# Optimization experiments

Hardware: AMD Instinct MI355X
Metric: run time of the kernel (lower is better)

## Reference

```python
import jax, jax.numpy as jnp
import numpy as np

# model geometry (matches init_kwargs cfg)
D = 768        # D_EMB
PATCH = 16
T = 8192
N = T // PATCH # 512 patch tokens
H = 12         # heads
HD = D // H    # 64 head dim
NL = 6         # layers
DFF = 4 * D
B = 8
LN_EPS = 1e-5


def setup_inputs() -> dict:
    key = jax.random.key(0)
    ks = iter(jax.random.split(key, 32))
    def g(shape, scale=0.02):
        return jax.random.normal(next(ks), shape, jnp.float32) * scale
    return dict(
        x=jax.random.normal(next(ks), (B, T), jnp.float32),
        pp_w=g((D, PATCH)), pp_b=jnp.zeros((D,), jnp.float32),
        pe=g((N, D)),
        ln1_g=jnp.ones((NL, D), jnp.float32), ln1_b=jnp.zeros((NL, D), jnp.float32),
        qkv_w=g((NL, 3 * D, D)), out_w=g((NL, D, D)),
        ln2_g=jnp.ones((NL, D), jnp.float32), ln2_b=jnp.zeros((NL, D), jnp.float32),
        fc1_w=g((NL, DFF, D)), fc2_w=g((NL, D, DFF)),
        lnf_g=jnp.ones((D,), jnp.float32), lnf_b=jnp.zeros((D,), jnp.float32),
        h1_w=g((D // 2, D)), h1_b=jnp.zeros((D // 2,), jnp.float32),
        h2_w=g((2, D // 2)), h2_b=jnp.zeros((2,), jnp.float32),
    )


def _ln(x, g, b):
    m = x.mean(-1, keepdims=True)
    v = ((x - m) ** 2).mean(-1, keepdims=True)
    return (x - m) / jnp.sqrt(v + LN_EPS) * g + b


def reference(x, pp_w, pp_b, pe, ln1_g, ln1_b, qkv_w, out_w,
              ln2_g, ln2_b, fc1_w, fc2_w, lnf_g, lnf_b,
              h1_w, h1_b, h2_w, h2_b):
    Bx = x.shape[0]
    # patch embed: [B, N, PATCH] @ W^T + b -> [B, N, D]
    z = jnp.einsum('bnp,dp->bnd', x[:, :N * PATCH].reshape(Bx, N, PATCH), pp_w) + pp_b
    z = z + pe  # positional embedding (arange indexes whole table)
    mask = jnp.tril(jnp.ones((N, N), dtype=bool))
    for i in range(NL):
        # --- attention (manual causal softmax, dropout=eval/no-op) ---
        h = _ln(z, ln1_g[i], ln1_b[i])
        qkv = jnp.einsum('bnd,ed->bne', h, qkv_w[i])            # [B,N,3D]
        qkv = qkv.reshape(Bx, N, 3, H, HD).transpose(2, 0, 3, 1, 4)
        q, k, v = qkv[0], qkv[1], qkv[2]                         # [B,H,N,HD]
        s = jnp.einsum('bhld,bhmd->bhlm', q, k) / np.sqrt(HD)
        s = jnp.where(mask, s, -jnp.inf)
        a = jax.nn.softmax(s, axis=-1)
        o = jnp.einsum('bhlm,bhmd->bhld', a, v)
        o = o.transpose(0, 2, 1, 3).reshape(Bx, N, D)
        z = z + jnp.einsum('bnd,ed->bne', o, out_w[i])
        # --- FFN (exact gelu, matching F.gelu default) ---
        h = _ln(z, ln2_g[i], ln2_b[i])
        f = jax.nn.gelu(jnp.einsum('bnd,fd->bnf', h, fc1_w[i]), approximate=False)
        z = z + jnp.einsum('bnf,df->bnd', f, fc2_w[i])
    enc = _ln(z, lnf_g, lnf_b).mean(axis=1)                      # [B, D]
    y = jax.nn.relu(enc @ h1_w.T + h1_b)
    return y @ h2_w.T + h2_b                                     # [B, 2]
```

## Files before the change

### kernel.cpp

```cpp
#include <hip/hip_runtime.h>
#include <hip/hip_bf16.h>
#include <math.h>

#define D_EMB 768
#define NPATCH 16
#define NTOK 512
#define NHEAD 12
#define HDIM 64
#define NLAYER 6
#define DFF 3072
#define BATCH 8
#define MTOK (BATCH * NTOK)

typedef __attribute__((ext_vector_type(8))) short bf16x8;
typedef __attribute__((ext_vector_type(4))) float f32x4;

__device__ __forceinline__ float bf2f(ushort s) {
    unsigned u = ((unsigned)s) << 16;
    return __builtin_bit_cast(float, u);
}
__device__ __forceinline__ ushort f2bf(float f) {
    unsigned u = __builtin_bit_cast(unsigned, f);
    unsigned r = (u + 0x7FFFu + ((u >> 16) & 1u)) >> 16;
    return (ushort)r;
}

__global__ __launch_bounds__(256)
void f2bf4_kernel(const float* __restrict__ s0, ushort* __restrict__ d0, int n0,
                  const float* __restrict__ s1, ushort* __restrict__ d1, int n1,
                  const float* __restrict__ s2, ushort* __restrict__ d2, int n2,
                  const float* __restrict__ s3, ushort* __restrict__ d3, int n3)
{
    int i = blockIdx.x * 256 + threadIdx.x;
    const float* s; ushort* d; int off;
    if (i < n0)                { s = s0; d = d0; off = i; }
    else if (i < n0 + n1)      { s = s1; d = d1; off = i - n0; }
    else if (i < n0 + n1 + n2) { s = s2; d = d2; off = i - n0 - n1; }
    else if (i < n0 + n1 + n2 + n3) { s = s3; d = d3; off = i - n0 - n1 - n2; }
    else return;
    float4 v = *(const float4*)(s + (size_t)off * 4);
    ushort4 o;
    o.x = f2bf(v.x); o.y = f2bf(v.y); o.z = f2bf(v.z); o.w = f2bf(v.w);
    *(ushort4*)(d + (size_t)off * 4) = o;
}

__global__ __launch_bounds__(256)
void patch_embed_kernel(const float* __restrict__ x, const float* __restrict__ pw,
                        const float* __restrict__ pb, const float* __restrict__ pe,
                        float* __restrict__ z)
{
    int bn = blockIdx.x;
    int b = bn >> 9, n = bn & 511;
    __shared__ float xs[NPATCH];
    int t = threadIdx.x;
    if (t < NPATCH) xs[t] = x[(size_t)b * 8192 + n * NPATCH + t];
    __syncthreads();
    for (int d = t; d < D_EMB; d += 256) {
        float acc = pb[d] + pe[(size_t)n * D_EMB + d];
        const float* w = pw + (size_t)d * NPATCH;
        #pragma unroll
        for (int p = 0; p < NPATCH; ++p) acc += xs[p] * w[p];
        z[(size_t)bn * D_EMB + d] = acc;
    }
}

__device__ __forceinline__ float block_reduce_sum_256(float v)
{
    __shared__ float lds[4];
    #pragma unroll
    for (int o = 32; o > 0; o >>= 1) v += __shfl_xor(v, o);
    int lane = threadIdx.x & 63, wid = threadIdx.x >> 6;
    __syncthreads();
    if (lane == 0) lds[wid] = v;
    __syncthreads();
    return lds[0] + lds[1] + lds[2] + lds[3];
}

__device__ __forceinline__ void store_val(float* p, float v)  { *p = v; }
__device__ __forceinline__ void store_val(ushort* p, float v) { *p = f2bf(v); }

template<typename OT>
__global__ __launch_bounds__(256)
void ln_kernel(const float* __restrict__ x, const float* __restrict__ g,
               const float* __restrict__ bta, OT* __restrict__ y)
{
    int row = blockIdx.x;
    const float* xr = x + (size_t)row * D_EMB;
    int t = threadIdx.x;
    float vals[3];
    float s = 0.f;
    #pragma unroll
    for (int i = 0; i < 3; ++i) { vals[i] = xr[t + i * 256]; s += vals[i]; }
    float mean = block_reduce_sum_256(s) * (1.0f / D_EMB);
    float ss = 0.f;
    #pragma unroll
    for (int i = 0; i < 3; ++i) { float d = vals[i] - mean; ss += d * d; }
    float var = block_reduce_sum_256(ss) * (1.0f / D_EMB);
    float rstd = rsqrtf(var + 1e-5f);
    #pragma unroll
    for (int i = 0; i < 3; ++i) {
        int d = t + i * 256;
        store_val(y + (size_t)row * D_EMB + d, (vals[i] - mean) * rstd * g[d] + bta[d]);
    }
}

template<typename OT>
__global__ __launch_bounds__(256)
void reduce_ln_kernel(const float* __restrict__ pbuf, float* __restrict__ z,
                      const float* __restrict__ g, const float* __restrict__ bta,
                      OT* __restrict__ y)
{
    int row = blockIdx.x;
    int t = threadIdx.x;
    const float* p0 = pbuf + (size_t)row * D_EMB;
    const float* p1 = pbuf + (size_t)MTOK * D_EMB + (size_t)row * D_EMB;
    float* zr = z + (size_t)row * D_EMB;
    float vals[3];
    float s = 0.f;
    #pragma unroll
    for (int i = 0; i < 3; ++i) {
        int d = t + i * 256;
        float v = zr[d] + p0[d] + p1[d];
        vals[i] = v;
        zr[d] = v;
        s += v;
    }
    float mean = block_reduce_sum_256(s) * (1.0f / D_EMB);
    float ss = 0.f;
    #pragma unroll
    for (int i = 0; i < 3; ++i) { float d = vals[i] - mean; ss += d * d; }
    float var = block_reduce_sum_256(ss) * (1.0f / D_EMB);
    float rstd = rsqrtf(var + 1e-5f);
    #pragma unroll
    for (int i = 0; i < 3; ++i) {
        int d = t + i * 256;
        store_val(y + (size_t)row * D_EMB + d, (vals[i] - mean) * rstd * g[d] + bta[d]);
    }
}

#define STAGE64(buf, k0)                                                           \
    {                                                                              \
        _Pragma("unroll")                                                          \
        for (int j = 0; j < 2; ++j) {                                              \
            int row = j * 32 + srow;                                               \
            int lcol = pcol ^ (row & 7);                                           \
            const ushort* sa = Ab + (size_t)(bm + row) * lda + (k0) + (lcol << 3); \
            __builtin_amdgcn_global_load_lds(                                      \
                (const __attribute__((address_space(1))) unsigned int*)sa,         \
                (__attribute__((address_space(3))) unsigned int*)&As[buf][row * 64 + (pcol << 3)], \
                16, 0, 0);                                                         \
        }                                                                          \
        _Pragma("unroll")                                                          \
        for (int j = 0; j < 4; ++j) {                                              \
            int row = j * 32 + srow;                                               \
            int lcol = pcol ^ (row & 7);                                           \
            const ushort* sb = Wb + (size_t)(bn + row) * lda + (k0) + (lcol << 3); \
            __builtin_amdgcn_global_load_lds(                                      \
                (const __attribute__((address_space(1))) unsigned int*)sb,         \
                (__attribute__((address_space(3))) unsigned int*)&Bs[buf][row * 64 + (pcol << 3)], \
                16, 0, 0);                                                         \
        }                                                                          \
    }

#define COMPUTE64(buf)                                                             \
    {                                                                              \
        _Pragma("unroll")                                                          \
        for (int kk = 0; kk < 2; ++kk) {                                           \
            int c = kk * 4 + lg;                                                   \
            bf16x8 a[4], b[2];                                                     \
            _Pragma("unroll")                                                      \
            for (int m = 0; m < 4; ++m) {                                          \
                int row = m * 16 + lr;                                             \
                a[m] = *(const bf16x8*)(&As[buf][row * 64 + ((c ^ (row & 7)) << 3)]); \
            }                                                                      \
            _Pragma("unroll")                                                      \
            for (int n = 0; n < 2; ++n) {                                          \
                int row = w * 32 + n * 16 + lr;                                    \
                b[n] = *(const bf16x8*)(&Bs[buf][row * 64 + ((c ^ (row & 7)) << 3)]); \
            }                                                                      \
            _Pragma("unroll")                                                      \
            for (int m = 0; m < 4; ++m) {                                          \
                _Pragma("unroll")                                                  \
                for (int n = 0; n < 2; ++n)                                        \
                    acc[m][n] = __builtin_amdgcn_mfma_f32_16x16x32_bf16(a[m], b[n], acc[m][n], 0, 0, 0); \
            }                                                                      \
        }                                                                          \
    }

template<int EPI, typename OT, bool SPLITK>
__global__ __launch_bounds__(256)
void mfma_gemm(const ushort* __restrict__ A, const ushort* __restrict__ W,
               OT* __restrict__ C, const float* __restrict__ res,
               int N, int K, int lda)
{
    __shared__ ushort As[2][64 * 64];
    __shared__ ushort Bs[2][128 * 64];

    int gx = gridDim.x, gy = gridDim.y;
    int bx = blockIdx.x, by = blockIdx.y;
    int bz = SPLITK ? blockIdx.z : 0;
    if ((gy & 7) == 0) {
        int flat = bx + gx * (by + gy * bz);
        int xcd = flat & 7, j = flat >> 3;
        int ry = gy >> 3;
        by = xcd * ry + (j % ry);
        int rem = j / ry;
        bx = rem % gx;
        bz = rem / gx;
    }
    int bm = by * 64, bn = bx * 128;

    const ushort* Ab = A + (size_t)bz * K;
    const ushort* Wb = W + (size_t)bz * K;
    OT* Cb = C + (SPLITK ? (size_t)bz * ((size_t)gy * 64) * N : 0);

    int tid = threadIdx.x;
    int w = tid >> 6, l = tid & 63;
    int lr = l & 15, lg = l >> 4;
    f32x4 acc[4][2] = {};

    int srow = w * 8 + (l >> 3);
    int pcol = l & 7;

    const int nk = K >> 6;
    STAGE64(0, 0);
    __syncthreads();
    int cur = 0;
    for (int t = 0; t < nk; ++t) {
        if (t + 1 < nk) STAGE64(cur ^ 1, (t + 1) << 6);
        COMPUTE64(cur);
        __syncthreads();
        cur ^= 1;
    }

    int r0 = lg * 4;
    #pragma unroll
    for (int m = 0; m < 4; ++m) {
        #pragma unroll
        for (int n = 0; n < 2; ++n) {
            #pragma unroll
            for (int j = 0; j < 4; ++j) {
                int gm = bm + m * 16 + r0 + j;
                int gn = bn + w * 32 + n * 16 + lr;
                float v = acc[m][n][j];
                if (EPI == 1) v = 0.5f * v * (1.0f + erff(v * 0.70710678118654752f));
                if (EPI == 2) v += res[(size_t)gm * N + gn];
                store_val(Cb + (size_t)gm * N + gn, v);
            }
        }
    }
}

__global__ __launch_bounds__(256)
void attn_mfma_kernel(const ushort* __restrict__ qkv, ushort* __restrict__ o)
{
    int w = threadIdx.x >> 6, l = threadIdx.x & 63;
    int qt = blockIdx.x * 4 + w;
    int h = blockIdx.y, b = blockIdx.z;
    int q0 = qt * 16;
    int lr = l & 15, lg = l >> 4;

    const size_t rs = 3 * D_EMB;
    const ushort* qbase = qkv + ((size_t)(b * NTOK)) * rs + h * HDIM;
    const ushort* kbase = qbase + D_EMB;
    const ushort* vbase = qbase + 2 * D_EMB;

    bf16x8 qf[2];
    qf[0] = *(const bf16x8*)(qbase + (size_t)(q0 + lr) * rs + lg * 8);
    qf[1] = *(const bf16x8*)(qbase + (size_t)(q0 + lr) * rs + 32 + lg * 8);

    f32x4 oacc[4] = {};
    float m_j[4], l_j[4];
    #pragma unroll
    for (int j = 0; j < 4; ++j) { m_j[j] = -1e30f; l_j[j] = 0.f; }

    __shared__ ushort P_lds[4][16][40];

    int ntiles = q0 / 32 + 1;
    for (int mt = 0; mt < ntiles; ++mt) {
        int m0 = mt * 32;
        f32x4 s[2] = {};
        #pragma unroll
        for (int kb = 0; kb < 2; ++kb) {
            const ushort* kr = kbase + (size_t)(m0 + kb * 16 + lr) * rs;
            bf16x8 k0 = *(const bf16x8*)(kr + lg * 8);
            bf16x8 k1 = *(const bf16x8*)(kr + 32 + lg * 8);
            s[kb] = __builtin_amdgcn_mfma_f32_16x16x32_bf16(qf[0], k0, s[kb], 0, 0, 0);
            s[kb] = __builtin_amdgcn_mfma_f32_16x16x32_bf16(qf[1], k1, s[kb], 0, 0, 0);
        }
        bool partial = (m0 + 31 > q0);
        float p[2][4], mx[4];
        #pragma unroll
        for (int j = 0; j < 4; ++j) {
            int qr = q0 + lg * 4 + j;
            float s0 = s[0][j] * 0.125f;
            float s1 = s[1][j] * 0.125f;
            if (partial) {
                if (m0 + lr > qr)      s0 = -1e30f;
                if (m0 + 16 + lr > qr) s1 = -1e30f;
            }
            p[0][j] = s0; p[1][j] = s1;
            float mm = fmaxf(s0, s1);
            mm = fmaxf(mm, __shfl_xor(mm, 1));
            mm = fmaxf(mm, __shfl_xor(mm, 2));
            mm = fmaxf(mm, __shfl_xor(mm, 4));
            mm = fmaxf(mm, __shfl_xor(mm, 8));
            mx[j] = mm;
        }
        #pragma unroll
        for (int j = 0; j < 4; ++j) {
            float mnew = fmaxf(m_j[j], mx[j]);
            float scale = __expf(m_j[j] - mnew);
            float p0 = __expf(p[0][j] - mnew);
            float p1 = __expf(p[1][j] - mnew);
            p[0][j] = p0; p[1][j] = p1;
            float rsum = p0 + p1;
            rsum += __shfl_xor(rsum, 1);
            rsum += __shfl_xor(rsum, 2);
            rsum += __shfl_xor(rsum, 4);
            rsum += __shfl_xor(rsum, 8);
            l_j[j] = l_j[j] * scale + rsum;
            m_j[j] = mnew;
            #pragma unroll
            for (int i = 0; i < 4; ++i) oacc[i][j] *= scale;
        }
        #pragma unroll
        for (int kb = 0; kb < 2; ++kb)
            #pragma unroll
            for (int j = 0; j < 4; ++j)
                P_lds[w][lg * 4 + j][kb * 16 + lr] = f2bf(p[kb][j]);
        asm volatile("s_waitcnt lgkmcnt(0)" ::: "memory");
        bf16x8 pa = *(const bf16x8*)(&P_lds[w][lr][lg * 8]);
        #pragma unroll
        for (int i = 0; i < 4; ++i) {
            bf16x8 vf;
            const ushort* vp = vbase + (size_t)(m0 + lg * 8) * rs + i * 16 + lr;
            #pragma unroll
            for (int j = 0; j < 8; ++j) vf[j] = (short)vp[(size_t)j * rs];
            oacc[i] = __builtin_amdgcn_mfma_f32_16x16x32_bf16(pa, vf, oacc[i], 0, 0, 0);
        }
    }
    #pragma unroll
    for (int i = 0; i < 4; ++i) {
        #pragma unroll
        for (int j = 0; j < 4; ++j) {
            int qr = q0 + lg * 4 + j;
            int d  = i * 16 + lr;
            float v = oacc[i][j] / l_j[j];
            o[((size_t)(b * NTOK + qr)) * D_EMB + h * HDIM + d] = f2bf(v);
        }
    }
}

__global__ void mean_kernel(const float* __restrict__ x, float* __restrict__ enc)
{
    int b = blockIdx.x; int d = threadIdx.x;
    float s = 0.f;
    for (int n = 0; n < NTOK; ++n) s += x[((size_t)(b * NTOK + n)) * D_EMB + d];
    enc[b * D_EMB + d] = s * (1.0f / NTOK);
}

__global__ void head1_kernel(const float* __restrict__ enc, const float* __restrict__ w,
                             const float* __restrict__ bias, float* __restrict__ r)
{
    int b = blockIdx.x; int j = threadIdx.x;
    float acc = bias[j];
    const float* e = enc + b * D_EMB;
    const float* wr = w + (size_t)j * D_EMB;
    for (int k = 0; k < D_EMB; ++k) acc += e[k] * wr[k];
    r[b * 384 + j] = fmaxf(acc, 0.f);
}

__global__ void head2_kernel(const float* __restrict__ r, const float* __restrict__ w,
                             const float* __restrict__ bias, float* __restrict__ out)
{
    int idx = threadIdx.x;
    if (idx >= 16) return;
    int b = idx >> 1, j = idx & 1;
    float acc = bias[j];
    for (int k = 0; k < 384; ++k) acc += r[b * 384 + k] * w[j * 384 + k];
    out[b * 2 + j] = acc;
}

extern "C" void kernel_launch(void* const* d_in, const int* in_sizes, int n_in,
                              void* d_out, int out_size, void* d_ws, size_t ws_size,
                              hipStream_t stream)
{
    const float* x     = (const float*)d_in[0];
    const float* pp_w  = (const float*)d_in[1];
    const float* pp_b  = (const float*)d_in[2];
    const float* pe    = (const float*)d_in[3];
    const float* ln1_g = (const float*)d_in[4];
    const float* ln1_b = (const float*)d_in[5];
    const float* qkv_w = (const float*)d_in[6];
    const float* out_w = (const float*)d_in[7];
    const float* ln2_g = (const float*)d_in[8];
    const float* ln2_b = (const float*)d_in[9];
    const float* fc1_w = (const float*)d_in[10];
    const float* fc2_w = (const float*)d_in[11];
    const float* lnf_g = (const float*)d_in[12];
    const float* lnf_b = (const float*)d_in[13];
    const float* h1_w  = (const float*)d_in[14];
    const float* h1_b  = (const float*)d_in[15];
    const float* h2_w  = (const float*)d_in[16];
    const float* h2_b  = (const float*)d_in[17];
    float* out = (float*)d_out;

    const int nq = 3 * D_EMB * D_EMB, no = D_EMB * D_EMB, nf = DFF * D_EMB;
    const size_t per_layer_w = ((size_t)nq + no + 2 * nf) * 2;

    char* p = (char*)d_ws;
    float*  z      = (float*)p;  p += (size_t)MTOK * D_EMB * 4;
    ushort* big_bf = (ushort*)p; p += (size_t)MTOK * DFF * 2;
    ushort* h_bf   = (ushort*)p; p += (size_t)MTOK * D_EMB * 2;
    float*  pbuf   = (float*)p;  p += (size_t)2 * MTOK * D_EMB * 4;
    float*  enc    = (float*)p;  p += BATCH * D_EMB * 4;
    float*  r1     = (float*)p;  p += BATCH * 384 * 4;
    size_t base_used = (size_t)(p - (char*)d_ws);
    bool full = (ws_size >= base_used + NLAYER * per_layer_w);
    int nlw = full ? NLAYER : 1;
    ushort* wq_bf  = (ushort*)p; p += (size_t)nlw * nq * 2;
    ushort* wo_bf  = (ushort*)p; p += (size_t)nlw * no * 2;
    ushort* wf1_bf = (ushort*)p; p += (size_t)nlw * nf * 2;
    ushort* wf2_bf = (ushort*)p; p += (size_t)nlw * nf * 2;
    float*  lnf_out = (float*)big_bf;

    patch_embed_kernel<<<MTOK, 256, 0, stream>>>(x, pp_w, pp_b, pe, z);

    if (full) {
        long long tq = (long long)NLAYER * nq / 4, to = (long long)NLAYER * no / 4;
        long long tf = (long long)NLAYER * nf / 4;
        long long tot = tq + to + 2 * tf;
        f2bf4_kernel<<<(int)((tot + 255) / 256), 256, 0, stream>>>(
            qkv_w, wq_bf, (int)tq, out_w, wo_bf, (int)to,
            fc1_w, wf1_bf, (int)tf, fc2_w, wf2_bf, (int)tf);
    }

    ln_kernel<ushort><<<MTOK, 256, 0, stream>>>(z, ln1_g, ln1_b, h_bf);

    const int cvt_blocks = (nq / 4 + no / 4 + 2 * (nf / 4) + 255) / 256;

    for (int i = 0; i < NLAYER; ++i) {
        const ushort* wq  = wq_bf  + (full ? (size_t)i * nq : 0);
        const ushort* wo  = wo_bf  + (full ? (size_t)i * no : 0);
        const ushort* wf1 = wf1_bf + (full ? (size_t)i * nf : 0);
        const ushort* wf2 = wf2_bf + (full ? (size_t)i * nf : 0);
        if (!full) {
            f2bf4_kernel<<<cvt_blocks, 256, 0, stream>>>(
                qkv_w + (size_t)i * nq, wq_bf,  nq / 4,
                out_w + (size_t)i * no, wo_bf,  no / 4,
                fc1_w + (size_t)i * nf, wf1_bf, nf / 4,
                fc2_w + (size_t)i * nf, wf2_bf, nf / 4);
        }

        dim3 gq((3 * D_EMB) / 128, MTOK / 64);
        mfma_gemm<0, ushort, false><<<gq, 256, 0, stream>>>(h_bf, wq, big_bf, nullptr,
                                                            3 * D_EMB, D_EMB, D_EMB);

        dim3 ga(NTOK / 64, NHEAD, BATCH);
        attn_mfma_kernel<<<ga, 256, 0, stream>>>(big_bf, h_bf);

        dim3 gp(D_EMB / 128, MTOK / 64);
        mfma_gemm<2, float, false><<<gp, 256, 0, stream>>>(h_bf, wo, z, z,
                                                           D_EMB, D_EMB, D_EMB);

        ln_kernel<ushort><<<MTOK, 256, 0, stream>>>(z, ln2_g + i * D_EMB, ln2_b + i * D_EMB, h_bf);

        dim3 g1(DFF / 128, MTOK / 64);
        mfma_gemm<1, ushort, false><<<g1, 256, 0, stream>>>(h_bf, wf1, big_bf, nullptr,
                                                            DFF, D_EMB, D_EMB);

        dim3 g2(D_EMB / 128, MTOK / 64, 2);
        mfma_gemm<0, float, true><<<g2, 256, 0, stream>>>(big_bf, wf2, pbuf, nullptr,
                                                          D_EMB, DFF / 2, DFF);

        if (i < NLAYER - 1) {
            reduce_ln_kernel<ushort><<<MTOK, 256, 0, stream>>>(
                pbuf, z, ln1_g + (i + 1) * D_EMB, ln1_b + (i + 1) * D_EMB, h_bf);
        } else {
            reduce_ln_kernel<float><<<MTOK, 256, 0, stream>>>(
                pbuf, z, lnf_g, lnf_b, lnf_out);
        }
    }

    mean_kernel<<<BATCH, D_EMB, 0, stream>>>(lnf_out, enc);
    head1_kernel<<<BATCH, 384, 0, stream>>>(enc, h1_w, h1_b, r1);
    head2_kernel<<<1, 64, 0, stream>>>(r1, h2_w, h2_b, out);
}
```

Baseline: 1.102 ms.

## Load GEMM operands directly from global into registers, widen weight conversion

The GEMM drops the double-buffered LDS staging (global_load_lds plus swizzled shared-memory reads and barriers). Each wave now loads its A and B MFMA fragments straight from global memory into registers and relies on L1/L2 to serve the overlap between waves. The fp32-to-bf16 weight conversion kernel is widened to handle 8 elements per thread. Dropping LDS removes the barriers and LDS traffic but loses the explicit prefetch and cross-wave reuse. The A tile is read by all four waves, so global/L2 traffic and load latency may go up.

```diff
diff --git a/kernel.cpp b/kernel.cpp
--- a/kernel.cpp
+++ b/kernel.cpp
@@ -13,6 +13,7 @@
 #define MTOK (BATCH * NTOK)
 
 typedef __attribute__((ext_vector_type(8))) short bf16x8;
+typedef __attribute__((ext_vector_type(8))) ushort u16x8;
 typedef __attribute__((ext_vector_type(4))) float f32x4;
 
 __device__ __forceinline__ float bf2f(ushort s) {
@@ -32,16 +33,18 @@
                   const float* __restrict__ s3, ushort* __restrict__ d3, int n3)
 {
     int i = blockIdx.x * 256 + threadIdx.x;
-    const float* s; ushort* d; int off;
+    const float* s; ushort* d; long long off;
     if (i < n0)                { s = s0; d = d0; off = i; }
     else if (i < n0 + n1)      { s = s1; d = d1; off = i - n0; }
     else if (i < n0 + n1 + n2) { s = s2; d = d2; off = i - n0 - n1; }
     else if (i < n0 + n1 + n2 + n3) { s = s3; d = d3; off = i - n0 - n1 - n2; }
     else return;
-    float4 v = *(const float4*)(s + (size_t)off * 4);
-    ushort4 o;
-    o.x = f2bf(v.x); o.y = f2bf(v.y); o.z = f2bf(v.z); o.w = f2bf(v.w);
-    *(ushort4*)(d + (size_t)off * 4) = o;
+    float4 v0 = *(const float4*)(s + off * 8);
+    float4 v1 = *(const float4*)(s + off * 8 + 4);
+    u16x8 o;
+    o[0] = f2bf(v0.x); o[1] = f2bf(v0.y); o[2] = f2bf(v0.z); o[3] = f2bf(v0.w);
+    o[4] = f2bf(v1.x); o[5] = f2bf(v1.y); o[6] = f2bf(v1.z); o[7] = f2bf(v1.w);
+    *(u16x8*)(d + off * 8) = o;
 }
 
 __global__ __launch_bounds__(256)
@@ -138,64 +141,12 @@
     }
 }
 
-#define STAGE64(buf, k0)                                                           \
-    {                                                                              \
-        _Pragma("unroll")                                                          \
-        for (int j = 0; j < 2; ++j) {                                              \
-            int row = j * 32 + srow;                                               \
-            int lcol = pcol ^ (row & 7);                                           \
-            const ushort* sa = Ab + (size_t)(bm + row) * lda + (k0) + (lcol << 3); \
-            __builtin_amdgcn_global_load_lds(                                      \
-                (const __attribute__((address_space(1))) unsigned int*)sa,         \
-                (__attribute__((address_space(3))) unsigned int*)&As[buf][row * 64 + (pcol << 3)], \
-                16, 0, 0);                                                         \
-        }                                                                          \
-        _Pragma("unroll")                                                          \
-        for (int j = 0; j < 4; ++j) {                                              \
-            int row = j * 32 + srow;                                               \
-            int lcol = pcol ^ (row & 7);                                           \
-            const ushort* sb = Wb + (size_t)(bn + row) * lda + (k0) + (lcol << 3); \
-            __builtin_amdgcn_global_load_lds(                                      \
-                (const __attribute__((address_space(1))) unsigned int*)sb,         \
-                (__attribute__((address_space(3))) unsigned int*)&Bs[buf][row * 64 + (pcol << 3)], \
-                16, 0, 0);                                                         \
-        }                                                                          \
-    }
-
-#define COMPUTE64(buf)                                                             \
-    {                                                                              \
-        _Pragma("unroll")                                                          \
-        for (int kk = 0; kk < 2; ++kk) {                                           \
-            int c = kk * 4 + lg;                                                   \
-            bf16x8 a[4], b[2];                                                     \
-            _Pragma("unroll")                                                      \
-            for (int m = 0; m < 4; ++m) {                                          \
-                int row = m * 16 + lr;                                             \
-                a[m] = *(const bf16x8*)(&As[buf][row * 64 + ((c ^ (row & 7)) << 3)]); \
-            }                                                                      \
-            _Pragma("unroll")                                                      \
-            for (int n = 0; n < 2; ++n) {                                          \
-                int row = w * 32 + n * 16 + lr;                                    \
-                b[n] = *(const bf16x8*)(&Bs[buf][row * 64 + ((c ^ (row & 7)) << 3)]); \
-            }                                                                      \
-            _Pragma("unroll")                                                      \
-            for (int m = 0; m < 4; ++m) {                                          \
-                _Pragma("unroll")                                                  \
-                for (int n = 0; n < 2; ++n)                                        \
-                    acc[m][n] = __builtin_amdgcn_mfma_f32_16x16x32_bf16(a[m], b[n], acc[m][n], 0, 0, 0); \
-            }                                                                      \
-        }                                                                          \
-    }
-
 template<int EPI, typename OT, bool SPLITK>
 __global__ __launch_bounds__(256)
 void mfma_gemm(const ushort* __restrict__ A, const ushort* __restrict__ W,
                OT* __restrict__ C, const float* __restrict__ res,
                int N, int K, int lda)
 {
-    __shared__ ushort As[2][64 * 64];
-    __shared__ ushort Bs[2][128 * 64];
-
     int gx = gridDim.x, gy = gridDim.y;
     int bx = blockIdx.x, by = blockIdx.y;
     int bz = SPLITK ? blockIdx.z : 0;
@@ -219,18 +170,33 @@
     int lr = l & 15, lg = l >> 4;
     f32x4 acc[4][2] = {};
 
-    int srow = w * 8 + (l >> 3);
-    int pcol = l & 7;
-
-    const int nk = K >> 6;
-    STAGE64(0, 0);
-    __syncthreads();
-    int cur = 0;
-    for (int t = 0; t < nk; ++t) {
-        if (t + 1 < nk) STAGE64(cur ^ 1, (t + 1) << 6);
-        COMPUTE64(cur);
-        __syncthreads();
-        cur ^= 1;
+    const ushort* pa0 = Ab + (size_t)(bm +  0 + lr) * lda + lg * 8;
+    const ushort* pa1 = Ab + (size_t)(bm + 16 + lr) * lda + lg * 8;
+    const ushort* pa2 = Ab + (size_t)(bm + 32 + lr) * lda + lg * 8;
+    const ushort* pa3 = Ab + (size_t)(bm + 48 + lr) * lda + lg * 8;
+    const ushort* pb0 = Wb + (size_t)(bn + w * 32 +  0 + lr) * lda + lg * 8;
+    const ushort* pb1 = Wb + (size_t)(bn + w * 32 + 16 + lr) * lda + lg * 8;
+
+    for (int k0 = 0; k0 < K; k0 += 64) {
+        bf16x8 a0[4], b0[2], a1[4], b1[2];
+        a0[0] = *(const bf16x8*)(pa0);      a1[0] = *(const bf16x8*)(pa0 + 32);
+        a0[1] = *(const bf16x8*)(pa1);      a1[1] = *(const bf16x8*)(pa1 + 32);
+        a0[2] = *(const bf16x8*)(pa2);      a1[2] = *(const bf16x8*)(pa2 + 32);
+        a0[3] = *(const bf16x8*)(pa3);      a1[3] = *(const bf16x8*)(pa3 + 32);
+        b0[0] = *(const bf16x8*)(pb0);      b1[0] = *(const bf16x8*)(pb0 + 32);
+        b0[1] = *(const bf16x8*)(pb1);      b1[1] = *(const bf16x8*)(pb1 + 32);
+        #pragma unroll
+        for (int m = 0; m < 4; ++m)
+            #pragma unroll
+            for (int n = 0; n < 2; ++n)
+                acc[m][n] = __builtin_amdgcn_mfma_f32_16x16x32_bf16(a0[m], b0[n], acc[m][n], 0, 0, 0);
+        #pragma unroll
+        for (int m = 0; m < 4; ++m)
+            #pragma unroll
+            for (int n = 0; n < 2; ++n)
+                acc[m][n] = __builtin_amdgcn_mfma_f32_16x16x32_bf16(a1[m], b1[n], acc[m][n], 0, 0, 0);
+        pa0 += 64; pa1 += 64; pa2 += 64; pa3 += 64;
+        pb0 += 64; pb1 += 64;
     }
 
     int r0 = lg * 4;
@@ -428,8 +394,8 @@
     patch_embed_kernel<<<MTOK, 256, 0, stream>>>(x, pp_w, pp_b, pe, z);
 
     if (full) {
-        long long tq = (long long)NLAYER * nq / 4, to = (long long)NLAYER * no / 4;
-        long long tf = (long long)NLAYER * nf / 4;
+        long long tq = (long long)NLAYER * nq / 8, to = (long long)NLAYER * no / 8;
+        long long tf = (long long)NLAYER * nf / 8;
         long long tot = tq + to + 2 * tf;
         f2bf4_kernel<<<(int)((tot + 255) / 256), 256, 0, stream>>>(
             qkv_w, wq_bf, (int)tq, out_w, wo_bf, (int)to,
@@ -438,7 +404,7 @@
 
     ln_kernel<ushort><<<MTOK, 256, 0, stream>>>(z, ln1_g, ln1_b, h_bf);
 
-    const int cvt_blocks = (nq / 4 + no / 4 + 2 * (nf / 4) + 255) / 256;
+    const int cvt_blocks = (nq / 8 + no / 8 + 2 * (nf / 8) + 255) / 256;
 
     for (int i = 0; i < NLAYER; ++i) {
         const ushort* wq  = wq_bf  + (full ? (size_t)i * nq : 0);
@@ -447,10 +413,10 @@
         const ushort* wf2 = wf2_bf + (full ? (size_t)i * nf : 0);
         if (!full) {
             f2bf4_kernel<<<cvt_blocks, 256, 0, stream>>>(
-                qkv_w + (size_t)i * nq, wq_bf,  nq / 4,
-                out_w + (size_t)i * no, wo_bf,  no / 4,
-                fc1_w + (size_t)i * nf, wf1_bf, nf / 4,
-                fc2_w + (size_t)i * nf, wf2_bf, nf / 4);
+                qkv_w + (size_t)i * nq, wq_bf,  nq / 8,
+                out_w + (size_t)i * no, wo_bf,  no / 8,
+                fc1_w + (size_t)i * nf, wf1_bf, nf / 8,
+                fc2_w + (size_t)i * nf, wf2_bf, nf / 8);
         }
 
         dim3 gq((3 * D_EMB) / 128, MTOK / 64);
```

New measurement: 2.405 ms. 2.18x slower.
